# Kernel optimization log

Measured on AMD Instinct MI355X. Metric: run time of the kernel, lower is better.

## Reference

```python
import jax, jax.numpy as jnp
import numpy as np

N_SRC, N_DST, N_EDGES = 200000, 100000, 600000
D_IN, D_OUT = 128, 128
NUM_EDGE_TYPES = 7
SCALING_FACTOR = 100.0


def setup_inputs() -> dict:
    key = jax.random.key(0)
    ks = jax.random.split(key, 6)
    x_src = jax.random.normal(ks[0], (N_SRC, D_IN), dtype=jnp.float32)
    x_target = jax.random.normal(ks[1], (N_DST, D_IN), dtype=jnp.float32)
    row = jax.random.randint(ks[2], (N_EDGES,), 0, N_SRC, dtype=jnp.int64 if jax.config.jax_enable_x64 else jnp.int32)
    col = jax.random.randint(ks[3], (N_EDGES,), 0, N_DST, dtype=jnp.int64 if jax.config.jax_enable_x64 else jnp.int32)
    edge_type = jax.random.randint(ks[4], (N_EDGES,), 0, NUM_EDGE_TYPES, dtype=jnp.int32)
    # Parameters (mirroring reset_parameters): xavier_uniform weight, zero bias,
    # relation_weight = 1/scaling_factor constant.
    limit = float(np.sqrt(6.0 / (D_IN + D_OUT)))
    weight = jax.random.uniform(ks[5], (D_IN, D_OUT), minval=-limit, maxval=limit, dtype=jnp.float32)
    bias = jnp.zeros((D_OUT,), dtype=jnp.float32)
    relation_weight = jnp.full((NUM_EDGE_TYPES,), 1.0 / SCALING_FACTOR, dtype=jnp.float32)
    return {"x_src": x_src, "x_target": x_target, "row": row, "col": col,
            "edge_type": edge_type, "weight": weight, "bias": bias,
            "relation_weight": relation_weight}


def reference(x_src, x_target, row, col, edge_type, weight, bias, relation_weight):
    n_dst = x_target.shape[0]
    # per-type linear transform (shared weight, applied to src and target)
    h_src = x_src @ weight                      # [N_src, D_out]
    h_tgt = x_target @ weight                   # [N_dst, D_out] (computed as in original; unused by 'add' aggr)
    # relation weights: one-hot(e_feat) @ leaky_relu(rw * s) == gather
    rw = jax.nn.leaky_relu(relation_weight * SCALING_FACTOR)
    edge_weight = rw[edge_type]                 # [E]
    # weighted in-degree normalization over destination nodes
    deg = jax.ops.segment_sum(edge_weight, col, num_segments=n_dst)  # [N_dst]
    ew = edge_weight / deg[col]                 # [E]
    # gather -> scale -> scatter-add message passing
    msg = ew[:, None] * h_src[row]              # [E, D_out]
    out = jnp.zeros((n_dst, h_src.shape[1]), dtype=h_src.dtype).at[col].add(msg)
    return out + bias
```

## Files before the change

kernel.cpp:

```cpp
#include <hip/hip_runtime.h>

#define D 128
#define CAP 64

typedef __attribute__((ext_vector_type(8))) short bf16x8;
typedef __attribute__((ext_vector_type(4))) float f32x4;
typedef __attribute__((ext_vector_type(8))) ushort ushort8;

struct EW { int r; float w; };

__device__ __forceinline__ float rel_w(const float* __restrict__ rel, int t) {
    float v = rel[t] * 100.0f;
    return v > 0.0f ? v : 0.01f * v;
}

__device__ __forceinline__ ushort f2b(float x) {
    unsigned u = __float_as_uint(x);
    u += 0x7FFFu + ((u >> 16) & 1u);
    return (ushort)(u >> 16);
}

__device__ __forceinline__ float b2f(ushort u) {
    return __uint_as_float((unsigned)u << 16);
}

__global__ void k_place(const int* __restrict__ col, const int* __restrict__ row,
                        const int* __restrict__ et, const float* __restrict__ rel,
                        int* __restrict__ cnt, EW* __restrict__ ewr,
                        const float* __restrict__ W, ushort* __restrict__ Wt, int ne) {
    const int e = blockIdx.x * blockDim.x + threadIdx.x;
    if (e < ne) {
        const int c = col[e];
        const int p = atomicAdd(&cnt[c], 1);
        if (p < CAP) {
            EW rec; rec.r = row[e]; rec.w = rel_w(rel, et[e]);
            ewr[(size_t)c * CAP + p] = rec;
        }
    }
    if (e < D * D) {
        const int n = e >> 7, k = e & 127;
        Wt[e] = f2b(W[k * D + n]);
    }
}

__global__ __launch_bounds__(256) void k_gemm(const float* __restrict__ X,
                                              const ushort* __restrict__ Wt,
                                              ushort* __restrict__ Hb, int nrows) {
    __shared__ ushort sW[D * 136];
    __shared__ ushort sA[64 * 136];
    const int t = threadIdx.x;
    const int rbase = blockIdx.x * 64;

    #pragma unroll
    for (int p = 0; p < 8; ++p) {
        const int idx = p * 2048 + t * 8;
        const int n = idx >> 7, k = idx & 127;
        *(bf16x8*)&sW[n * 136 + k] = *(const bf16x8*)&Wt[idx];
    }
    #pragma unroll
    for (int p = 0; p < 4; ++p) {
        const int idx = p * 2048 + t * 8;
        const int r = idx >> 7, k = idx & 127;
        const int gr = rbase + r;
        ushort8 v = {};
        if (gr < nrows) {
            const float4 xa = *(const float4*)&X[(size_t)gr * D + k];
            const float4 xb = *(const float4*)&X[(size_t)gr * D + k + 4];
            v[0] = f2b(xa.x); v[1] = f2b(xa.y); v[2] = f2b(xa.z); v[3] = f2b(xa.w);
            v[4] = f2b(xb.x); v[5] = f2b(xb.y); v[6] = f2b(xb.z); v[7] = f2b(xb.w);
        }
        *(ushort8*)&sA[r * 136 + k] = v;
    }
    __syncthreads();

    const int w = t >> 6, l = t & 63;
    const int m16 = l & 15, g4 = l >> 4;
    const int arow = w * 16 + m16;

    f32x4 acc[8] = {};
    #pragma unroll
    for (int ks = 0; ks < 4; ++ks) {
        const int k0 = ks * 32 + g4 * 8;
        const bf16x8 a = *(const bf16x8*)&sA[arow * 136 + k0];
        #pragma unroll
        for (int nf = 0; nf < 8; ++nf) {
            const bf16x8 b = *(const bf16x8*)&sW[(nf * 16 + m16) * 136 + k0];
            acc[nf] = __builtin_amdgcn_mfma_f32_16x16x32_bf16(a, b, acc[nf], 0, 0, 0);
        }
    }

    #pragma unroll
    for (int nf = 0; nf < 8; ++nf) {
        const int colj = nf * 16 + m16;
        #pragma unroll
        for (int q = 0; q < 4; ++q) {
            const int r = rbase + w * 16 + g4 * 4 + q;
            if (r < nrows) Hb[(size_t)r * D + colj] = f2b(acc[nf][q]);
        }
    }
}

__global__ __launch_bounds__(256) void k_agg(const ushort* __restrict__ Hb,
                                             const EW* __restrict__ ewr,
                                             const int* __restrict__ cnt,
                                             const float* __restrict__ bias,
                                             float* __restrict__ out, int ndst) {
    const int dw = (int)((blockIdx.x * blockDim.x + threadIdx.x) >> 6);
    const int lane = threadIdx.x & 63;
    if (dw >= ndst) return;
    const int c = min(cnt[dw], CAP);
    const int m16 = lane & 15, g4 = lane >> 4;

    EW e0; e0.r = 0; e0.w = 0.f;
    if (lane < c) e0 = ewr[(size_t)dw * CAP + lane];

    float wsum = e0.w;
    #pragma unroll
    for (int s = 1; s < 64; s <<= 1) wsum += __shfl_xor(wsum, s);
    const float inv = (wsum != 0.f) ? 1.f / wsum : 0.f;

    const int r0 = e0.r; const float wv = e0.w * inv;
    float acc[8] = {};
    for (int j0 = 0; j0 < c; j0 += 4) {
        const int j = j0 + g4;
        const int   rr = __shfl(r0, j);
        const float ww = __shfl(wv, j);
        const ushort8 hv = *(const ushort8*)&Hb[(size_t)rr * D + m16 * 8];
        #pragma unroll
        for (int i = 0; i < 8; ++i)
            acc[i] = fmaf(ww, b2f(hv[i]), acc[i]);
    }

    #pragma unroll
    for (int i = 0; i < 8; ++i) {
        acc[i] += __shfl_xor(acc[i], 16);
        acc[i] += __shfl_xor(acc[i], 32);
    }

    if (lane < 16) {
        const float4 b0 = *(const float4*)&bias[m16 * 8];
        const float4 b1 = *(const float4*)&bias[m16 * 8 + 4];
        float4 o0, o1;
        o0.x = acc[0] + b0.x; o0.y = acc[1] + b0.y;
        o0.z = acc[2] + b0.z; o0.w = acc[3] + b0.w;
        o1.x = acc[4] + b1.x; o1.y = acc[5] + b1.y;
        o1.z = acc[6] + b1.z; o1.w = acc[7] + b1.w;
        *(float4*)&out[(size_t)dw * D + m16 * 8]     = o0;
        *(float4*)&out[(size_t)dw * D + m16 * 8 + 4] = o1;
    }
}

extern "C" void kernel_launch(void* const* d_in, const int* in_sizes, int n_in,
                              void* d_out, int out_size, void* d_ws, size_t ws_size,
                              hipStream_t stream) {
    const float* x_src  = (const float*)d_in[0];
    const int*   row    = (const int*)d_in[2];
    const int*   col    = (const int*)d_in[3];
    const int*   etype  = (const int*)d_in[4];
    const float* weight = (const float*)d_in[5];
    const float* bias   = (const float*)d_in[6];
    const float* relw   = (const float*)d_in[7];

    const int nsrc = in_sizes[0] / D;
    const int ndst = out_size / D;
    const int ne   = in_sizes[2];

    ushort* Hb  = (ushort*)d_ws;
    ushort* Wt  = Hb + (size_t)nsrc * D;
    EW*     ewr = (EW*)(Wt + D * D);
    int*    cnt = (int*)(ewr + (size_t)ndst * CAP);

    float* out = (float*)d_out;

    hipMemsetAsync(cnt, 0, (size_t)ndst * sizeof(int), stream);
    hipLaunchKernelGGL(k_place, dim3((ne + 255) / 256), dim3(256), 0, stream,
                       col, row, etype, relw, cnt, ewr, weight, Wt, ne);
    hipLaunchKernelGGL(k_gemm, dim3((nsrc + 63) / 64), dim3(256), 0, stream,
                       x_src, Wt, Hb, nsrc);
    hipLaunchKernelGGL(k_agg, dim3((ndst + 3) / 4), dim3(256), 0, stream,
                       Hb, ewr, cnt, bias, out, ndst);
}
```

Measured before the change: 111.1 us.

## Fuse edge placement into GEMM launch and replace memset with init kernel

Replaces the memset with a small init kernel that zeroes the per-destination counters and transposes the weight to bf16. The edge bucketing work now runs as extra blocks inside the GEMM kernel, selected by block index. This removes one launch and lets the atomic-heavy placement overlap with the compute-bound GEMM. The placement blocks still reserve the GEMM's large static shared memory, which can limit how many of them are resident at once.

```diff
diff --git a/kernel.cpp b/kernel.cpp
--- a/kernel.cpp
+++ b/kernel.cpp
@@ -24,31 +24,42 @@
     return __uint_as_float((unsigned)u << 16);
 }
 
-__global__ void k_place(const int* __restrict__ col, const int* __restrict__ row,
-                        const int* __restrict__ et, const float* __restrict__ rel,
-                        int* __restrict__ cnt, EW* __restrict__ ewr,
-                        const float* __restrict__ W, ushort* __restrict__ Wt, int ne) {
-    const int e = blockIdx.x * blockDim.x + threadIdx.x;
-    if (e < ne) {
-        const int c = col[e];
-        const int p = atomicAdd(&cnt[c], 1);
-        if (p < CAP) {
-            EW rec; rec.r = row[e]; rec.w = rel_w(rel, et[e]);
-            ewr[(size_t)c * CAP + p] = rec;
-        }
-    }
-    if (e < D * D) {
-        const int n = e >> 7, k = e & 127;
-        Wt[e] = f2b(W[k * D + n]);
+__global__ void k_init(int* __restrict__ cnt, const float* __restrict__ W,
+                       ushort* __restrict__ Wt, int ndst) {
+    const int i = blockIdx.x * blockDim.x + threadIdx.x;
+    if (i < ndst) cnt[i] = 0;
+    if (i < D * D) {
+        const int n = i >> 7, k = i & 127;
+        Wt[i] = f2b(W[k * D + n]);
     }
 }
 
-__global__ __launch_bounds__(256) void k_gemm(const float* __restrict__ X,
-                                              const ushort* __restrict__ Wt,
-                                              ushort* __restrict__ Hb, int nrows) {
+__global__ __launch_bounds__(256) void k_fused(const float* __restrict__ X,
+                                               const ushort* __restrict__ Wt,
+                                               ushort* __restrict__ Hb, int nrows,
+                                               const int* __restrict__ col,
+                                               const int* __restrict__ row,
+                                               const int* __restrict__ et,
+                                               const float* __restrict__ rel,
+                                               int* __restrict__ cnt,
+                                               EW* __restrict__ ewr, int ne, int nbg) {
     __shared__ ushort sW[D * 136];
     __shared__ ushort sA[64 * 136];
     const int t = threadIdx.x;
+
+    if (blockIdx.x >= nbg) {
+        const int e = (blockIdx.x - nbg) * blockDim.x + t;
+        if (e < ne) {
+            const int c = col[e];
+            const int p = atomicAdd(&cnt[c], 1);
+            if (p < CAP) {
+                EW rec; rec.r = row[e]; rec.w = rel_w(rel, et[e]);
+                ewr[(size_t)c * CAP + p] = rec;
+            }
+        }
+        return;
+    }
+
     const int rbase = blockIdx.x * 64;
 
     #pragma unroll
@@ -172,11 +183,14 @@
 
     float* out = (float*)d_out;
 
-    hipMemsetAsync(cnt, 0, (size_t)ndst * sizeof(int), stream);
-    hipLaunchKernelGGL(k_place, dim3((ne + 255) / 256), dim3(256), 0, stream,
-                       col, row, etype, relw, cnt, ewr, weight, Wt, ne);
-    hipLaunchKernelGGL(k_gemm, dim3((nsrc + 63) / 64), dim3(256), 0, stream,
-                       x_src, Wt, Hb, nsrc);
+    const int nbg = (nsrc + 63) / 64;
+    const int nbe = (ne + 255) / 256;
+    const int ninit = max(ndst, D * D);
+
+    hipLaunchKernelGGL(k_init, dim3((ninit + 255) / 256), dim3(256), 0, stream,
+                       cnt, weight, Wt, ndst);
+    hipLaunchKernelGGL(k_fused, dim3(nbg + nbe), dim3(256), 0, stream,
+                       x_src, Wt, Hb, nsrc, col, row, etype, relw, cnt, ewr, ne, nbg);
     hipLaunchKernelGGL(k_agg, dim3((ndst + 3) / 4), dim3(256), 0, stream,
                        Hb, ewr, cnt, bias, out, ndst);
 }
```

After: 108.6 us. 1.02x faster.
